# Kernel optimization log

Hardware: AMD Instinct MI355X
Metric: run time of the kernel (lower is better)

The kernel has to match this reference:

```python
import jax, jax.numpy as jnp
import numpy as np

N_NODES = 100000
N_EDGES = 1600000
DIM_IN = 128
DIM_OUT = 128


def setup_inputs() -> dict:
    key = jax.random.key(0)
    k1, k2, k3, k4, k5 = jax.random.split(key, 5)
    x = jax.random.normal(k1, (N_NODES, DIM_IN), dtype=jnp.float32)
    W = jax.random.normal(k2, (DIM_OUT, DIM_IN), dtype=jnp.float32) * (1.0 / np.sqrt(DIM_IN))
    vals = jax.random.uniform(k3, (N_EDGES,), dtype=jnp.float32)
    src = jax.random.randint(k4, (N_EDGES,), 0, N_NODES, dtype=jnp.int32)
    dst = jax.random.randint(k5, (N_EDGES,), 0, N_NODES, dtype=jnp.int32)
    return {"x": x, "W": W, "vals": vals, "src": src, "dst": dst}


def reference(x, W, vals, src, dst):
    # Linear projection (nn.Linear with bias=False): h = x @ W^T  -> [N, dim_out]
    h = jnp.einsum('nd,od->no', x, W)
    # Sparse adjacency SpMM in COO form: out[i] = sum_{e: dst[e]==i} vals[e] * h[src[e]]
    msgs = vals[:, None] * h[src]  # [E, dim_out] irregular gather
    out = jax.ops.segment_sum(msgs, dst, num_segments=N_NODES)  # [N, dim_out] scatter-add
    return out
```

## Files before the change

### kernel.cpp

```cpp
#include <hip/hip_runtime.h>

#define N_NODES 100000
#define N_EDGES 1600000
#define DIM 128

#define NPB 64
#define NBUCK 1563
#define EPB 4096
#define NBLK_E 391
#define NBLK_G 1563
#define NBLK_M 782

#define OFF_H       0
#define OFF_BCNT    25600000
#define OFF_BBASE   25606272
#define OFF_BCUR    25612544
#define OFF_EPACK   25618816
#define OFF_ROWPTR  38418816
#define OFF_WPL     38818944
#define WS_NEED     38884480

typedef __attribute__((ext_vector_type(8))) __bf16 bf16x8;
typedef __attribute__((ext_vector_type(4))) float  f32x4;

union U4B8 { uint4 u; bf16x8 v; };
union B8   { __bf16 b[8]; bf16x8 v; };

static __device__ __forceinline__ unsigned short f2bf(float f) {
    union { float f; unsigned u; } a; a.f = f;
    unsigned r = a.u + 0x7fffu + ((a.u >> 16) & 1u);
    return (unsigned short)(r >> 16);
}

static __device__ __forceinline__ float bf2f(unsigned short h) {
    return __uint_as_float((unsigned)h << 16);
}

static __device__ __forceinline__ float bflo(unsigned b) {
    return __uint_as_float(b << 16);
}
static __device__ __forceinline__ float bfhi(unsigned b) {
    return __uint_as_float(b & 0xffff0000u);
}

__global__ __launch_bounds__(256) void zero_out_kernel(float4* __restrict__ out) {
    int i = blockIdx.x * 256 + threadIdx.x;
    if (i < N_NODES * DIM / 4) out[i] = make_float4(0.f, 0.f, 0.f, 0.f);
}

__global__ __launch_bounds__(256) void prep_kernel(
        const float4* __restrict__ W4, unsigned* __restrict__ wpl,
        int* __restrict__ bcnt)
{
    const int b = blockIdx.x;
    if (b < 16) {
        int idx = b * 256 + threadIdx.x;
        int j   = idx >> 5;
        int c4  = idx & 31;
        float4 v = W4[idx];
        unsigned short hx = f2bf(v.x), hy = f2bf(v.y);
        unsigned short hz = f2bf(v.z), hw = f2bf(v.w);
        unsigned short lx = f2bf(v.x - bf2f(hx));
        unsigned short ly = f2bf(v.y - bf2f(hy));
        unsigned short lz = f2bf(v.z - bf2f(hz));
        unsigned short lw = f2bf(v.w - bf2f(hw));
        int dg = c4 * 2;
        int kc = dg >> 5;
        int dl = dg & 31;
        int p  = dl ^ ((j & 7) << 2);
        int base = kc * 8192 + j * 32;
        wpl[base + p]            = (unsigned)hx | ((unsigned)hy << 16);
        wpl[base + p + 1]        = (unsigned)hz | ((unsigned)hw << 16);
        wpl[base + 4096 + p]     = (unsigned)lx | ((unsigned)ly << 16);
        wpl[base + 4096 + p + 1] = (unsigned)lz | ((unsigned)lw << 16);
    } else {
        int i = (b - 16) * 256 + threadIdx.x;
        if (i < NBUCK) bcnt[i] = 0;
    }
}

#define GMR 128
__global__ __launch_bounds__(256) void gemm_mfma_kernel(
        const float4* __restrict__ x4,
        const unsigned* __restrict__ wpl,
        unsigned short* __restrict__ hb16)
{
    __shared__ alignas(16) unsigned lw[8192];

    const int t    = threadIdx.x;
    const int lane = t & 63;
    const int w    = t >> 6;
    const int col  = lane & 15;
    const int kg   = lane >> 4;
    const int r0   = blockIdx.x * GMR;

    const int arow0 = r0 + (w << 4) + col;
    const int arow1 = arow0 + 64;
    const bool ok0 = arow0 < N_NODES;
    const bool ok1 = arow1 < N_NODES;

    f32x4 acc[2][8];
#pragma unroll
    for (int rt = 0; rt < 2; ++rt)
#pragma unroll
        for (int jt = 0; jt < 8; ++jt) acc[rt][jt] = (f32x4)(0.f);

    for (int kc = 0; kc < 2; ++kc) {
        const uint4* g = (const uint4*)(wpl + kc * 8192);
#pragma unroll
        for (int i = 0; i < 8; ++i)
            ((uint4*)lw)[t + 256 * i] = g[t + 256 * i];
        __syncthreads();

#pragma unroll
        for (int kh = 0; kh < 2; ++kh) {
            const int ks = kc * 2 + kh;

            B8 ah[2], al[2];
#pragma unroll
            for (int rt = 0; rt < 2; ++rt) {
                float4 a0 = make_float4(0.f, 0.f, 0.f, 0.f);
                float4 a1 = make_float4(0.f, 0.f, 0.f, 0.f);
                const int arow = rt ? arow1 : arow0;
                const bool ok  = rt ? ok1 : ok0;
                if (ok) {
                    a0 = x4[(size_t)arow * 32 + ks * 8 + kg * 2];
                    a1 = x4[(size_t)arow * 32 + ks * 8 + kg * 2 + 1];
                }
                float av[8] = {a0.x, a0.y, a0.z, a0.w, a1.x, a1.y, a1.z, a1.w};
#pragma unroll
                for (int e = 0; e < 8; ++e) {
                    __bf16 h = (__bf16)av[e];
                    ah[rt].b[e] = h;
                    al[rt].b[e] = (__bf16)(av[e] - (float)h);
                }
            }

            const int d0 = (kh << 4) + (kg << 2);
#pragma unroll
            for (int jt = 0; jt < 8; ++jt) {
                int j  = (jt << 4) + col;
                int p0 = d0 ^ ((j & 7) << 2);
                U4B8 bh, bl;
                bh.u = *(const uint4*)&lw[j * 32 + p0];
                bl.u = *(const uint4*)&lw[4096 + j * 32 + p0];
                acc[0][jt] = __builtin_amdgcn_mfma_f32_16x16x32_bf16(ah[0].v, bh.v, acc[0][jt], 0, 0, 0);
                acc[0][jt] = __builtin_amdgcn_mfma_f32_16x16x32_bf16(al[0].v, bh.v, acc[0][jt], 0, 0, 0);
                acc[0][jt] = __builtin_amdgcn_mfma_f32_16x16x32_bf16(ah[0].v, bl.v, acc[0][jt], 0, 0, 0);
                acc[1][jt] = __builtin_amdgcn_mfma_f32_16x16x32_bf16(ah[1].v, bh.v, acc[1][jt], 0, 0, 0);
                acc[1][jt] = __builtin_amdgcn_mfma_f32_16x16x32_bf16(al[1].v, bh.v, acc[1][jt], 0, 0, 0);
                acc[1][jt] = __builtin_amdgcn_mfma_f32_16x16x32_bf16(ah[1].v, bl.v, acc[1][jt], 0, 0, 0);
            }
        }
        __syncthreads();
    }

#pragma unroll
    for (int rt = 0; rt < 2; ++rt) {
#pragma unroll
        for (int jt = 0; jt < 8; ++jt) {
#pragma unroll
            for (int r = 0; r < 4; ++r) {
                int node = r0 + rt * 64 + (w << 4) + kg * 4 + r;
                if (node < N_NODES)
                    hb16[(size_t)node * 128 + (jt << 4) + col] = f2bf(acc[rt][jt][r]);
            }
        }
    }
}

__global__ __launch_bounds__(256) void bucket_hist_kernel(
        const int* __restrict__ dst, int* __restrict__ bcnt)
{
    __shared__ int lh[NBUCK];
    const int t = threadIdx.x;
    const int e0 = blockIdx.x * EPB;

    for (int i = t; i < NBUCK; i += 256) lh[i] = 0;
    __syncthreads();
#pragma unroll
    for (int r = 0; r < 16; ++r) {
        int e = e0 + (r << 8) + t;
        if (e < N_EDGES) atomicAdd(&lh[dst[e] >> 6], 1);
    }
    __syncthreads();
    const int phase = (blockIdx.x * 613) % NBUCK;
    for (int k = t; k < NBUCK; k += 256) {
        int i = k + phase; if (i >= NBUCK) i -= NBUCK;
        int c = lh[i];
        if (c) atomicAdd(&bcnt[i], c);
    }
}

__global__ __launch_bounds__(256) void bucket_scan_kernel(
        const int* __restrict__ bcnt, int* __restrict__ bbase,
        int* __restrict__ bcur)
{
    __shared__ int wsh[4];
    const int t = threadIdx.x, lane = t & 63, wv = t >> 6;
    int c[8]; int s = 0;
#pragma unroll
    for (int i = 0; i < 8; ++i) {
        int idx = t * 8 + i;
        c[i] = (idx < NBUCK) ? bcnt[idx] : 0;
        s += c[i];
    }
    int v = s;
#pragma unroll
    for (int off = 1; off < 64; off <<= 1) {
        int u = __shfl_up(v, off, 64);
        if (lane >= off) v += u;
    }
    if (lane == 63) wsh[wv] = v;
    __syncthreads();
    int we = 0;
#pragma unroll
    for (int w = 0; w < 4; ++w) we += (w < wv) ? wsh[w] : 0;
    int run = we + (v - s);
#pragma unroll
    for (int i = 0; i < 8; ++i) {
        int idx = t * 8 + i;
        if (idx < NBUCK) { bbase[idx] = run; bcur[idx] = run; }
        run += c[i];
    }
    if (t == 0) bbase[NBUCK] = N_EDGES;
}

__global__ __launch_bounds__(256) void bucket_fill_kernel(
        const int* __restrict__ src, const int* __restrict__ dst,
        const float* __restrict__ vals,
        int* __restrict__ bcur, uint2* __restrict__ ep)
{
    __shared__ int lh[NBUCK];
    __shared__ int lbase[NBUCK];
    const int t = threadIdx.x;
    const int e0 = blockIdx.x * EPB;

    for (int i = t; i < NBUCK; i += 256) lh[i] = 0;
    __syncthreads();
#pragma unroll
    for (int r = 0; r < 16; ++r) {
        int e = e0 + (r << 8) + t;
        if (e < N_EDGES) atomicAdd(&lh[dst[e] >> 6], 1);
    }
    __syncthreads();
    const int phase = (blockIdx.x * 613) % NBUCK;
    for (int k = t; k < NBUCK; k += 256) {
        int i = k + phase; if (i >= NBUCK) i -= NBUCK;
        int c = lh[i];
        lbase[i] = c ? atomicAdd(&bcur[i], c) : 0;
        lh[i] = 0;
    }
    __syncthreads();
#pragma unroll
    for (int r = 0; r < 16; ++r) {
        int e = e0 + (r << 8) + t;
        if (e < N_EDGES) {
            int d  = dst[e];
            int bk = d >> 6;
            int p  = lbase[bk] + atomicAdd(&lh[bk], 1);
            ep[p] = make_uint2((unsigned)src[e] | ((unsigned)(d & 63) << 17),
                               __float_as_uint(vals[e]));
        }
    }
}

__global__ __launch_bounds__(256) void reorder_kernel(
        const int* __restrict__ bbase,
        uint2* __restrict__ ep,
        int* __restrict__ row_ptr)
{
    __shared__ int lcnt[NPB];
    const int t = threadIdx.x;
    const int lane = t & 63;
    const int wv = t >> 6;
    const int b = blockIdx.x;

    const int jb = bbase[b];
    const int je = bbase[b + 1];
    const int cnt = je - jb;

    uint2 e[8];
#pragma unroll
    for (int r = 0; r < 8; ++r) {
        int idx = t + (r << 8);
        if (idx < cnt) e[r] = ep[jb + idx];
    }
    if (t < NPB) lcnt[t] = 0;
    __syncthreads();
#pragma unroll
    for (int r = 0; r < 8; ++r) {
        int idx = t + (r << 8);
        if (idx < cnt) atomicAdd(&lcnt[e[r].x >> 17], 1);
    }
    __syncthreads();
    if (wv == 0) {
        int c = lcnt[lane];
        int v = c;
#pragma unroll
        for (int off = 1; off < 64; off <<= 1) {
            int u = __shfl_up(v, off, 64);
            if (lane >= off) v += u;
        }
        int excl = v - c;
        lcnt[lane] = excl;
        int node = b * NPB + lane;
        if (node <= N_NODES) row_ptr[node] = jb + excl;
    }
    __syncthreads();
#pragma unroll
    for (int r = 0; r < 8; ++r) {
        int idx = t + (r << 8);
        if (idx < cnt) {
            int p = atomicAdd(&lcnt[e[r].x >> 17], 1);
            ep[jb + p] = make_uint2(e[r].x & 0x1FFFFu, e[r].y);
        }
    }
}

__global__ __launch_bounds__(256) void gather_bf16_kernel(
        const unsigned int* __restrict__ hbits,
        const int* __restrict__ row_ptr,
        const uint2* __restrict__ ep,
        float2* __restrict__ out2)
{
    const int lane = threadIdx.x & 63;
    const int node = blockIdx.x * 4 + (threadIdx.x >> 6);
    if (node >= N_NODES) return;

    const int jb = row_ptr[node];
    const int je = row_ptr[node + 1];

    float ax0 = 0.f, ay0 = 0.f, ax1 = 0.f, ay1 = 0.f;
    float ax2 = 0.f, ay2 = 0.f, ax3 = 0.f, ay3 = 0.f;
    float ax4 = 0.f, ay4 = 0.f, ax5 = 0.f, ay5 = 0.f;
    float ax6 = 0.f, ay6 = 0.f, ax7 = 0.f, ay7 = 0.f;

    int j = jb;
    if ((j & 1) && j < je) {
        uint2 e0 = ep[j];
        unsigned b0 = hbits[((size_t)e0.x << 6) + lane];
        float v0 = __uint_as_float(e0.y);
        ax0 += v0 * bflo(b0);
        ay0 += v0 * bfhi(b0);
        ++j;
    }
    for (; j + 7 < je; j += 8) {
        uint4 q0 = *(const uint4*)(ep + j);
        uint4 q1 = *(const uint4*)(ep + j + 2);
        uint4 q2 = *(const uint4*)(ep + j + 4);
        uint4 q3 = *(const uint4*)(ep + j + 6);
        unsigned b0 = hbits[((size_t)q0.x << 6) + lane];
        unsigned b1 = hbits[((size_t)q0.z << 6) + lane];
        unsigned b2 = hbits[((size_t)q1.x << 6) + lane];
        unsigned b3 = hbits[((size_t)q1.z << 6) + lane];
        unsigned b4 = hbits[((size_t)q2.x << 6) + lane];
        unsigned b5 = hbits[((size_t)q2.z << 6) + lane];
        unsigned b6 = hbits[((size_t)q3.x << 6) + lane];
        unsigned b7 = hbits[((size_t)q3.z << 6) + lane];
        float v0 = __uint_as_float(q0.y), v1 = __uint_as_float(q0.w);
        float v2 = __uint_as_float(q1.y), v3 = __uint_as_float(q1.w);
        float v4 = __uint_as_float(q2.y), v5 = __uint_as_float(q2.w);
        float v6 = __uint_as_float(q3.y), v7 = __uint_as_float(q3.w);
        ax0 += v0 * bflo(b0); ay0 += v0 * bfhi(b0);
        ax1 += v1 * bflo(b1); ay1 += v1 * bfhi(b1);
        ax2 += v2 * bflo(b2); ay2 += v2 * bfhi(b2);
        ax3 += v3 * bflo(b3); ay3 += v3 * bfhi(b3);
        ax4 += v4 * bflo(b4); ay4 += v4 * bfhi(b4);
        ax5 += v5 * bflo(b5); ay5 += v5 * bfhi(b5);
        ax6 += v6 * bflo(b6); ay6 += v6 * bfhi(b6);
        ax7 += v7 * bflo(b7); ay7 += v7 * bfhi(b7);
    }
    for (; j + 1 < je; j += 2) {
        uint4 q0 = *(const uint4*)(ep + j);
        unsigned b0 = hbits[((size_t)q0.x << 6) + lane];
        unsigned b1 = hbits[((size_t)q0.z << 6) + lane];
        float v0 = __uint_as_float(q0.y), v1 = __uint_as_float(q0.w);
        ax0 += v0 * bflo(b0); ay0 += v0 * bfhi(b0);
        ax1 += v1 * bflo(b1); ay1 += v1 * bfhi(b1);
    }
    if (j < je) {
        uint2 e0 = ep[j];
        unsigned b0 = hbits[((size_t)e0.x << 6) + lane];
        float v0 = __uint_as_float(e0.y);
        ax0 += v0 * bflo(b0);
        ay0 += v0 * bfhi(b0);
    }
    float sx = ((ax0 + ax1) + (ax2 + ax3)) + ((ax4 + ax5) + (ax6 + ax7));
    float sy = ((ay0 + ay1) + (ay2 + ay3)) + ((ay4 + ay5) + (ay6 + ay7));
    out2[(size_t)node * 64 + lane] = make_float2(sx, sy);
}

#define GR 64
__global__ __launch_bounds__(256) void gemm_tiled_kernel(
        const float4* __restrict__ x4, const float4* __restrict__ W4,
        unsigned int* __restrict__ hbits)
{
    __shared__ alignas(16) float xs[GR][68];
    __shared__ alignas(16) float wsh[64][132];

    const int t  = threadIdx.x;
    const int tx = t & 15;
    const int ty = t >> 4;
    const int r0 = blockIdx.x * GR;

    float acc[4][8];
#pragma unroll
    for (int i = 0; i < 4; ++i)
#pragma unroll
        for (int j = 0; j < 8; ++j) acc[i][j] = 0.f;

    for (int kc = 0; kc < 2; ++kc) {
#pragma unroll
        for (int i = 0; i < 4; ++i) {
            int linear = t + 256 * i;
            int r  = linear >> 4;
            int k4 = linear & 15;
            float4 v = make_float4(0.f, 0.f, 0.f, 0.f);
            if (r0 + r < N_NODES) v = x4[(size_t)(r0 + r) * 32 + kc * 16 + k4];
            *(float4*)&xs[r][k4 * 4] = v;
        }
#pragma unroll
        for (int i = 0; i < 8; ++i) {
            int linear = t + 256 * i;
            int c  = linear >> 4;
            int k4 = linear & 15;
            float4 v = W4[(size_t)c * 32 + kc * 16 + k4];
            wsh[k4 * 4 + 0][c] = v.x;
            wsh[k4 * 4 + 1][c] = v.y;
            wsh[k4 * 4 + 2][c] = v.z;
            wsh[k4 * 4 + 3][c] = v.w;
        }
        __syncthreads();
#pragma unroll 4
        for (int kk = 0; kk < 64; ++kk) {
            float xf[4], wf[8];
#pragma unroll
            for (int i = 0; i < 4; ++i) xf[i] = xs[ty * 4 + i][kk];
            float4 wlo4 = *(const float4*)&wsh[kk][tx * 8];
            float4 whi4 = *(const float4*)&wsh[kk][tx * 8 + 4];
            wf[0] = wlo4.x; wf[1] = wlo4.y; wf[2] = wlo4.z; wf[3] = wlo4.w;
            wf[4] = whi4.x; wf[5] = whi4.y; wf[6] = whi4.z; wf[7] = whi4.w;
#pragma unroll
            for (int i = 0; i < 4; ++i)
#pragma unroll
                for (int j = 0; j < 8; ++j) acc[i][j] += xf[i] * wf[j];
        }
        __syncthreads();
    }
#pragma unroll
    for (int i = 0; i < 4; ++i) {
        int r = r0 + ty * 4 + i;
        if (r < N_NODES) {
            uint4 u;
            u.x = (unsigned)f2bf(acc[i][0]) | ((unsigned)f2bf(acc[i][1]) << 16);
            u.y = (unsigned)f2bf(acc[i][2]) | ((unsigned)f2bf(acc[i][3]) << 16);
            u.z = (unsigned)f2bf(acc[i][4]) | ((unsigned)f2bf(acc[i][5]) << 16);
            u.w = (unsigned)f2bf(acc[i][6]) | ((unsigned)f2bf(acc[i][7]) << 16);
            *(uint4*)&hbits[(size_t)r * 64 + tx * 4] = u;
        }
    }
}

__global__ __launch_bounds__(256) void scatter_kernel(
        const unsigned int* __restrict__ hbits, const float* __restrict__ vals,
        const int* __restrict__ src, const int* __restrict__ dst,
        float* __restrict__ out)
{
    const int lane = threadIdx.x & 63;
    int e = (blockIdx.x * 256 + threadIdx.x) >> 6;
    if (e >= N_EDGES) return;
    const int   s = src[e];
    const int   d = dst[e];
    const float v = vals[e];
    unsigned b = hbits[(size_t)s * 64 + lane];
    float* op = out + (size_t)d * DIM + lane * 2;
    atomicAdd(op + 0, v * bflo(b));
    atomicAdd(op + 1, v * bfhi(b));
}

extern "C" void kernel_launch(void* const* d_in, const int* in_sizes, int n_in,
                              void* d_out, int out_size, void* d_ws, size_t ws_size,
                              hipStream_t stream) {
    const float* x    = (const float*)d_in[0];
    const float* W    = (const float*)d_in[1];
    const float* vals = (const float*)d_in[2];
    const int*   src  = (const int*)d_in[3];
    const int*   dst  = (const int*)d_in[4];
    float* out = (float*)d_out;

    char* ws = (char*)d_ws;
    unsigned* hbits = (unsigned*)(ws + OFF_H);
    int*   bcnt    = (int*)(ws + OFF_BCNT);
    int*   bbase   = (int*)(ws + OFF_BBASE);
    int*   bcur    = (int*)(ws + OFF_BCUR);
    uint2* ep      = (uint2*)(ws + OFF_EPACK);
    int*   row_ptr = (int*)(ws + OFF_ROWPTR);
    unsigned* wpl  = (unsigned*)(ws + OFF_WPL);

    if (ws_size >= (size_t)WS_NEED) {
        prep_kernel<<<16 + 7, 256, 0, stream>>>((const float4*)W, wpl, bcnt);
        bucket_hist_kernel<<<NBLK_E, 256, 0, stream>>>(dst, bcnt);
        bucket_scan_kernel<<<1, 256, 0, stream>>>(bcnt, bbase, bcur);
        gemm_mfma_kernel<<<NBLK_M, 256, 0, stream>>>(
            (const float4*)x, wpl, (unsigned short*)hbits);
        bucket_fill_kernel<<<NBLK_E, 256, 0, stream>>>(src, dst, vals, bcur, ep);
        reorder_kernel<<<NBUCK, 256, 0, stream>>>(bbase, ep, row_ptr);
        gather_bf16_kernel<<<(N_NODES + 3) / 4, 256, 0, stream>>>(
            hbits, row_ptr, ep, (float2*)out);
    } else {
        gemm_tiled_kernel<<<NBLK_G, 256, 0, stream>>>(
            (const float4*)x, (const float4*)W, hbits);
        zero_out_kernel<<<(N_NODES * DIM / 4 + 255) / 256, 256, 0, stream>>>((float4*)out);
        scatter_kernel<<<(N_EDGES * 64 + 255) / 256, 256, 0, stream>>>(
            hbits, vals, src, dst, out);
    }
}
```

Baseline: 269.3 us.

## Merge GEMM and bucket-fill into one launch with role-split blocks

Combines the MFMA projection GEMM and the edge bucket-fill pass into a single kernel, where the first blocks do the edge fill and the rest do the GEMM, reusing one shared-memory buffer. The aim is to drop a launch boundary and let the memory-bound fill run alongside the compute-bound GEMM. The gather kernel also moves its row_ptr bounds into scalar registers via readfirstlane. In exchange, occupancy is limited by the larger shared allocation for the fill blocks, and the two workloads now compete for the same CUs.

```diff
diff --git a/kernel.cpp b/kernel.cpp
--- a/kernel.cpp
+++ b/kernel.cpp
@@ -79,20 +79,119 @@
     }
 }
 
+__global__ __launch_bounds__(256) void bucket_hist_kernel(
+        const int* __restrict__ dst, int* __restrict__ bcnt)
+{
+    __shared__ int lh[NBUCK];
+    const int t = threadIdx.x;
+    const int e0 = blockIdx.x * EPB;
+
+    for (int i = t; i < NBUCK; i += 256) lh[i] = 0;
+    __syncthreads();
+#pragma unroll
+    for (int r = 0; r < 16; ++r) {
+        int e = e0 + (r << 8) + t;
+        if (e < N_EDGES) atomicAdd(&lh[dst[e] >> 6], 1);
+    }
+    __syncthreads();
+    const int phase = (blockIdx.x * 613) % NBUCK;
+    for (int k = t; k < NBUCK; k += 256) {
+        int i = k + phase; if (i >= NBUCK) i -= NBUCK;
+        int c = lh[i];
+        if (c) atomicAdd(&bcnt[i], c);
+    }
+}
+
+__global__ __launch_bounds__(256) void bucket_scan_kernel(
+        const int* __restrict__ bcnt, int* __restrict__ bbase,
+        int* __restrict__ bcur)
+{
+    __shared__ int wsh[4];
+    const int t = threadIdx.x, lane = t & 63, wv = t >> 6;
+    int c[8]; int s = 0;
+#pragma unroll
+    for (int i = 0; i < 8; ++i) {
+        int idx = t * 8 + i;
+        c[i] = (idx < NBUCK) ? bcnt[idx] : 0;
+        s += c[i];
+    }
+    int v = s;
+#pragma unroll
+    for (int off = 1; off < 64; off <<= 1) {
+        int u = __shfl_up(v, off, 64);
+        if (lane >= off) v += u;
+    }
+    if (lane == 63) wsh[wv] = v;
+    __syncthreads();
+    int we = 0;
+#pragma unroll
+    for (int w = 0; w < 4; ++w) we += (w < wv) ? wsh[w] : 0;
+    int run = we + (v - s);
+#pragma unroll
+    for (int i = 0; i < 8; ++i) {
+        int idx = t * 8 + i;
+        if (idx < NBUCK) { bbase[idx] = run; bcur[idx] = run; }
+        run += c[i];
+    }
+    if (t == 0) bbase[NBUCK] = N_EDGES;
+}
+
 #define GMR 128
-__global__ __launch_bounds__(256) void gemm_mfma_kernel(
+__global__ __launch_bounds__(256) void gemm_fill_kernel(
         const float4* __restrict__ x4,
         const unsigned* __restrict__ wpl,
-        unsigned short* __restrict__ hb16)
-{
-    __shared__ alignas(16) unsigned lw[8192];
-
-    const int t    = threadIdx.x;
+        unsigned short* __restrict__ hb16,
+        const int* __restrict__ src,
+        const int* __restrict__ dst,
+        const float* __restrict__ vals,
+        int* __restrict__ bcur,
+        uint2* __restrict__ ep)
+{
+    __shared__ alignas(16) unsigned smem[8192];
+    const int t = threadIdx.x;
+
+    if (blockIdx.x < NBLK_E) {
+        int* lh    = (int*)smem;
+        int* lbase = (int*)smem + NBUCK;
+        const int e0 = blockIdx.x * EPB;
+
+        for (int i = t; i < NBUCK; i += 256) lh[i] = 0;
+        __syncthreads();
+#pragma unroll
+        for (int r = 0; r < 16; ++r) {
+            int e = e0 + (r << 8) + t;
+            if (e < N_EDGES) atomicAdd(&lh[dst[e] >> 6], 1);
+        }
+        __syncthreads();
+        const int phase = (blockIdx.x * 613) % NBUCK;
+        for (int k = t; k < NBUCK; k += 256) {
+            int i = k + phase; if (i >= NBUCK) i -= NBUCK;
+            int c = lh[i];
+            lbase[i] = c ? atomicAdd(&bcur[i], c) : 0;
+            lh[i] = 0;
+        }
+        __syncthreads();
+#pragma unroll
+        for (int r = 0; r < 16; ++r) {
+            int e = e0 + (r << 8) + t;
+            if (e < N_EDGES) {
+                int d  = dst[e];
+                int bk = d >> 6;
+                int p  = lbase[bk] + atomicAdd(&lh[bk], 1);
+                ep[p] = make_uint2((unsigned)src[e] | ((unsigned)(d & 63) << 17),
+                                   __float_as_uint(vals[e]));
+            }
+        }
+        return;
+    }
+
+    unsigned* lw = smem;
+
     const int lane = t & 63;
     const int w    = t >> 6;
     const int col  = lane & 15;
     const int kg   = lane >> 4;
-    const int r0   = blockIdx.x * GMR;
+    const int r0   = (blockIdx.x - NBLK_E) * GMR;
 
     const int arow0 = r0 + (w << 4) + col;
     const int arow1 = arow0 + 64;
@@ -169,102 +268,6 @@
     }
 }
 
-__global__ __launch_bounds__(256) void bucket_hist_kernel(
-        const int* __restrict__ dst, int* __restrict__ bcnt)
-{
-    __shared__ int lh[NBUCK];
-    const int t = threadIdx.x;
-    const int e0 = blockIdx.x * EPB;
-
-    for (int i = t; i < NBUCK; i += 256) lh[i] = 0;
-    __syncthreads();
-#pragma unroll
-    for (int r = 0; r < 16; ++r) {
-        int e = e0 + (r << 8) + t;
-        if (e < N_EDGES) atomicAdd(&lh[dst[e] >> 6], 1);
-    }
-    __syncthreads();
-    const int phase = (blockIdx.x * 613) % NBUCK;
-    for (int k = t; k < NBUCK; k += 256) {
-        int i = k + phase; if (i >= NBUCK) i -= NBUCK;
-        int c = lh[i];
-        if (c) atomicAdd(&bcnt[i], c);
-    }
-}
-
-__global__ __launch_bounds__(256) void bucket_scan_kernel(
-        const int* __restrict__ bcnt, int* __restrict__ bbase,
-        int* __restrict__ bcur)
-{
-    __shared__ int wsh[4];
-    const int t = threadIdx.x, lane = t & 63, wv = t >> 6;
-    int c[8]; int s = 0;
-#pragma unroll
-    for (int i = 0; i < 8; ++i) {
-        int idx = t * 8 + i;
-        c[i] = (idx < NBUCK) ? bcnt[idx] : 0;
-        s += c[i];
-    }
-    int v = s;
-#pragma unroll
-    for (int off = 1; off < 64; off <<= 1) {
-        int u = __shfl_up(v, off, 64);
-        if (lane >= off) v += u;
-    }
-    if (lane == 63) wsh[wv] = v;
-    __syncthreads();
-    int we = 0;
-#pragma unroll
-    for (int w = 0; w < 4; ++w) we += (w < wv) ? wsh[w] : 0;
-    int run = we + (v - s);
-#pragma unroll
-    for (int i = 0; i < 8; ++i) {
-        int idx = t * 8 + i;
-        if (idx < NBUCK) { bbase[idx] = run; bcur[idx] = run; }
-        run += c[i];
-    }
-    if (t == 0) bbase[NBUCK] = N_EDGES;
-}
-
-__global__ __launch_bounds__(256) void bucket_fill_kernel(
-        const int* __restrict__ src, const int* __restrict__ dst,
-        const float* __restrict__ vals,
-        int* __restrict__ bcur, uint2* __restrict__ ep)
-{
-    __shared__ int lh[NBUCK];
-    __shared__ int lbase[NBUCK];
-    const int t = threadIdx.x;
-    const int e0 = blockIdx.x * EPB;
-
-    for (int i = t; i < NBUCK; i += 256) lh[i] = 0;
-    __syncthreads();
-#pragma unroll
-    for (int r = 0; r < 16; ++r) {
-        int e = e0 + (r << 8) + t;
-        if (e < N_EDGES) atomicAdd(&lh[dst[e] >> 6], 1);
-    }
-    __syncthreads();
-    const int phase = (blockIdx.x * 613) % NBUCK;
-    for (int k = t; k < NBUCK; k += 256) {
-        int i = k + phase; if (i >= NBUCK) i -= NBUCK;
-        int c = lh[i];
-        lbase[i] = c ? atomicAdd(&bcur[i], c) : 0;
-        lh[i] = 0;
-    }
-    __syncthreads();
-#pragma unroll
-    for (int r = 0; r < 16; ++r) {
-        int e = e0 + (r << 8) + t;
-        if (e < N_EDGES) {
-            int d  = dst[e];
-            int bk = d >> 6;
-            int p  = lbase[bk] + atomicAdd(&lh[bk], 1);
-            ep[p] = make_uint2((unsigned)src[e] | ((unsigned)(d & 63) << 17),
-                               __float_as_uint(vals[e]));
-        }
-    }
-}
-
 __global__ __launch_bounds__(256) void reorder_kernel(
         const int* __restrict__ bbase,
         uint2* __restrict__ ep,
@@ -328,8 +331,8 @@
     const int node = blockIdx.x * 4 + (threadIdx.x >> 6);
     if (node >= N_NODES) return;
 
-    const int jb = row_ptr[node];
-    const int je = row_ptr[node + 1];
+    const int jb = __builtin_amdgcn_readfirstlane(row_ptr[node]);
+    const int je = __builtin_amdgcn_readfirstlane(row_ptr[node + 1]);
 
     float ax0 = 0.f, ay0 = 0.f, ax1 = 0.f, ay1 = 0.f;
     float ax2 = 0.f, ay2 = 0.f, ax3 = 0.f, ay3 = 0.f;
@@ -502,9 +505,9 @@
         prep_kernel<<<16 + 7, 256, 0, stream>>>((const float4*)W, wpl, bcnt);
         bucket_hist_kernel<<<NBLK_E, 256, 0, stream>>>(dst, bcnt);
         bucket_scan_kernel<<<1, 256, 0, stream>>>(bcnt, bbase, bcur);
-        gemm_mfma_kernel<<<NBLK_M, 256, 0, stream>>>(
-            (const float4*)x, wpl, (unsigned short*)hbits);
-        bucket_fill_kernel<<<NBLK_E, 256, 0, stream>>>(src, dst, vals, bcur, ep);
+        gemm_fill_kernel<<<NBLK_E + NBLK_M, 256, 0, stream>>>(
+            (const float4*)x, wpl, (unsigned short*)hbits,
+            src, dst, vals, bcur, ep);
         reorder_kernel<<<NBUCK, 256, 0, stream>>>(bbase, ep, row_ptr);
         gather_bf16_kernel<<<(N_NODES + 3) / 4, 256, 0, stream>>>(
             hbits, row_ptr, ep, (float2*)out);
```

Measured after the change: 253.2 us. -6.0%, faster.
